# Kernel optimization log

Measured on AMD Instinct MI355X. Metric: run time of the kernel, lower is better.

The kernel has to match this reference:

```python
import jax, jax.numpy as jnp
import numpy as np

EPS = 1e-5


def bn(x, g, b, m, v):
    # eval-mode BatchNorm2d: x [B,C,H,W], params [C]
    s = g / jnp.sqrt(v + EPS)
    return x * s[None, :, None, None] + (b - m * s)[None, :, None, None]


def conv1x1(x, w):
    # x [B,C,H,W], w [O,C]
    return jnp.einsum('bchw,oc->bohw', x, w)


def offset_conv(x, w, b):
    # 3x3 conv, stride 1, pad 1, with bias; x [B,C,H,W], w [18,C,3,3]
    y = jax.lax.conv_general_dilated(x, w, window_strides=(1, 1),
                                     padding=((1, 1), (1, 1)),
                                     dimension_numbers=('NCHW', 'OIHW', 'NCHW'))
    return y + b[None, :, None, None]


def deform_conv3x3(x, offset, w):
    # DeformConv v1: x [B,C,H,W], offset [B,18,H,W] ((dy,dx) pairs per kernel
    # point, torchvision layout), w [O,C,3,3]; stride=1, pad=1, dil=1.
    B, C, H, W = x.shape
    oy = offset[:, 0::2]  # [B,9,H,W]
    ox = offset[:, 1::2]  # [B,9,H,W]
    kgy = (jnp.arange(9) // 3 - 1).astype(x.dtype)  # kernel y offsets
    kgx = (jnp.arange(9) % 3 - 1).astype(x.dtype)   # kernel x offsets
    hh = jnp.arange(H, dtype=x.dtype)
    ww = jnp.arange(W, dtype=x.dtype)
    py = hh[None, None, :, None] + kgy[None, :, None, None] + oy  # [B,9,H,W]
    px = ww[None, None, None, :] + kgx[None, :, None, None] + ox  # [B,9,H,W]
    feat = jnp.transpose(x, (0, 2, 3, 1))  # [B,H,W,C]
    y0 = jnp.floor(py)
    x0 = jnp.floor(px)
    wy = py - y0
    wx = px - x0
    bidx = jnp.arange(B).reshape(B, 1, 1, 1)
    acc = jnp.zeros((B, 9, H, W, C), dtype=x.dtype)
    for dy in (0, 1):
        for dx in (0, 1):
            yi = y0 + dy
            xi = x0 + dx
            wgt = (wy if dy else 1.0 - wy) * (wx if dx else 1.0 - wx)
            valid = (yi >= 0) & (yi <= H - 1) & (xi >= 0) & (xi <= W - 1)
            yic = jnp.clip(yi, 0, H - 1).astype(jnp.int32)
            xic = jnp.clip(xi, 0, W - 1).astype(jnp.int32)
            g = feat[bidx, yic, xic]  # gather -> [B,9,H,W,C]
            acc = acc + (wgt * valid.astype(x.dtype))[..., None] * g
    wk = w.reshape(w.shape[0], C, 9)  # k = ky*3+kx matches kgy/kgx order
    return jnp.einsum('bkhwc,ock->bohw', acc, wk)


def setup_inputs() -> dict:
    key = jax.random.key(0)
    ks = jax.random.split(key, 20)
    B, Cin, H, W = 16, 1024, 32, 32
    P, O = 256, 1024  # width / outplanes
    f32 = jnp.float32
    d = {}
    d['x'] = jax.random.normal(ks[0], (B, Cin, H, W), f32)
    d['w1'] = jax.random.normal(ks[1], (P, Cin), f32) * 0.02
    d['bn1_g'] = 1.0 + 0.1 * jax.random.normal(ks[2], (P,), f32)
    d['bn1_b'] = 0.1 * jax.random.normal(ks[3], (P,), f32)
    d['bn1_m'] = 0.1 * jax.random.normal(ks[4], (P,), f32)
    d['bn1_v'] = 0.5 + jax.random.uniform(ks[5], (P,), f32)
    d['off_w'] = jax.random.normal(ks[6], (18, P, 3, 3), f32) * 0.01
    d['off_b'] = 0.01 * jax.random.normal(ks[7], (18,), f32)
    d['w2'] = jax.random.normal(ks[8], (P, P, 3, 3), f32) * 0.02
    d['bn2_g'] = 1.0 + 0.1 * jax.random.normal(ks[9], (P,), f32)
    d['bn2_b'] = 0.1 * jax.random.normal(ks[10], (P,), f32)
    d['bn2_m'] = 0.1 * jax.random.normal(ks[11], (P,), f32)
    d['bn2_v'] = 0.5 + jax.random.uniform(ks[12], (P,), f32)
    d['w3'] = jax.random.normal(ks[13], (O, P), f32) * 0.02
    d['bn3_g'] = 1.0 + 0.1 * jax.random.normal(ks[14], (O,), f32)
    d['bn3_b'] = 0.1 * jax.random.normal(ks[15], (O,), f32)
    d['bn3_m'] = 0.1 * jax.random.normal(ks[16], (O,), f32)
    d['bn3_v'] = 0.5 + jax.random.uniform(ks[17], (O,), f32)
    return d


def reference(x, w1, bn1_g, bn1_b, bn1_m, bn1_v, off_w, off_b, w2,
              bn2_g, bn2_b, bn2_m, bn2_v, w3, bn3_g, bn3_b, bn3_m, bn3_v):
    shortcut = x
    h = jax.nn.relu(bn(conv1x1(x, w1), bn1_g, bn1_b, bn1_m, bn1_v))
    offset = offset_conv(h, off_w, off_b)
    h = deform_conv3x3(h, offset, w2)
    h = jax.nn.relu(bn(h, bn2_g, bn2_b, bn2_m, bn2_v))
    h = bn(conv1x1(h, w3), bn3_g, bn3_b, bn3_m, bn3_v)
    return jax.nn.relu(h + shortcut)
```

## Files before the change

### kernel.cpp

```cpp
#include <hip/hip_runtime.h>

#define BN_EPS 1e-5f

typedef __bf16 bf16_t;
typedef __bf16 bf16x8 __attribute__((ext_vector_type(8)));
typedef float f32x4 __attribute__((ext_vector_type(4)));


__global__ void __launch_bounds__(1024) k_bnprep(
    const float* g1, const float* b1, const float* m1, const float* v1,
    const float* g2, const float* b2, const float* m2, const float* v2,
    const float* g3, const float* b3, const float* m3, const float* v3,
    float* bnc) {
    int t = threadIdx.x;
    if (t < 256) {
        float s = g1[t] * rsqrtf(v1[t] + BN_EPS);
        bnc[t] = s;
        bnc[256 + t] = b1[t] - m1[t] * s;
        float s2 = g2[t] * rsqrtf(v2[t] + BN_EPS);
        bnc[512 + t] = s2;
        bnc[768 + t] = b2[t] - m2[t] * s2;
    }
    float s3 = g3[t] * rsqrtf(v3[t] + BN_EPS);
    bnc[1024 + t] = s3;
    bnc[2048 + t] = b3[t] - m3[t] * s3;
}

__global__ void __launch_bounds__(256) k_cast(const float* __restrict__ s,
                                              bf16_t* __restrict__ d, int n4) {
    int i = blockIdx.x * 256 + threadIdx.x;
    if (i >= n4) return;
    float4 v = ((const float4*)s)[i];
    d[4 * i + 0] = (bf16_t)v.x;
    d[4 * i + 1] = (bf16_t)v.y;
    d[4 * i + 2] = (bf16_t)v.z;
    d[4 * i + 3] = (bf16_t)v.w;
}

__global__ void __launch_bounds__(256) k_w2b(const float* __restrict__ w2,
                                             bf16_t* __restrict__ w2t) {
    int i = blockIdx.x * 256 + threadIdx.x;
    int o = i / 2304;
    int r = i - o * 2304;
    int kk = r >> 8;
    int c = r & 255;
    w2t[i] = (bf16_t)w2[(size_t)o * 2304 + c * 9 + kk];
}

__global__ void __launch_bounds__(256) k_owtb(const float* __restrict__ ow,
                                              bf16_t* __restrict__ owtb) {
    int idx = blockIdx.x * 256 + threadIdx.x;
    if (idx >= 73728) return;
    int j = idx / 2304;
    int rem = idx - j * 2304;
    int kp = rem >> 8;
    int c = rem & 255;
    float v = (j < 18) ? ow[(j * 256 + c) * 9 + kp] : 0.f;
    owtb[idx] = (bf16_t)v;
}

__global__ void __launch_bounds__(256) k_xb(const float* __restrict__ x,
                                            bf16_t* __restrict__ xb) {
    __shared__ float ld[64 * 68];
    int t = threadIdx.x;
    int hw0 = blockIdx.x * 64, c0 = blockIdx.y * 64, b = blockIdx.z;
    int ci = t >> 2, h0 = (t & 3) * 16;
    const float* src = x + ((size_t)(b * 1024 + c0 + ci) << 10) + hw0 + h0;
#pragma unroll
    for (int i = 0; i < 4; ++i)
        *(float4*)(ld + ci * 68 + h0 + 4 * i) = *(const float4*)(src + 4 * i);
    __syncthreads();
    int r = t >> 2, cc0 = (t & 3) * 16;
    bf16x8 o0, o1;
#pragma unroll
    for (int i = 0; i < 8; ++i) o0[i] = (bf16_t)ld[(cc0 + i) * 68 + r];
#pragma unroll
    for (int i = 0; i < 8; ++i) o1[i] = (bf16_t)ld[(cc0 + 8 + i) * 68 + r];
    bf16_t* dst = xb + ((size_t)(b * 1024 + hw0 + r) << 10) + c0 + cc0;
    *(bf16x8*)dst = o0;
    *(bf16x8*)(dst + 8) = o1;
}

__global__ void __launch_bounds__(256) k_gemm64(
    const bf16_t* __restrict__ A, const bf16_t* __restrict__ Bt, int K, int ldo,
    const float* __restrict__ sc, const float* __restrict__ sh,
    const float* __restrict__ resid, bf16_t* __restrict__ outb,
    float* __restrict__ outf, int epi) {
    __shared__ __align__(16) bf16_t As[64 * 40];
    __shared__ __align__(16) bf16_t Bs[128 * 40];
    int t = threadIdx.x;
    int lane = t & 63;
    int w = t >> 6;
    int wm = w >> 1, wn = w & 1;
    int m0 = blockIdx.x * 64, n0 = blockIdx.y * 128;

    int ar = t >> 2, as_ = t & 3;
    const bf16_t* ag = A + (size_t)(m0 + ar) * K + as_ * 8;
    int aw = ar * 40 + ((as_ ^ (ar & 3)) * 8);
    int bn0 = t >> 2, bs_ = t & 3;
    const bf16_t* bg0 = Bt + (size_t)(n0 + bn0) * K + bs_ * 8;
    const bf16_t* bg1 = Bt + (size_t)(n0 + 64 + bn0) * K + bs_ * 8;
    int bw0 = bn0 * 40 + ((bs_ ^ (bn0 & 3)) * 8);
    int bw1 = (64 + bn0) * 40 + ((bs_ ^ (bn0 & 3)) * 8);

    int asel = lane >> 4;
    int ar0 = wm * 32 + (lane & 15);
    int aoff0 = ar0 * 40 + ((asel ^ (ar0 & 3)) * 8);
    int aoff1 = (ar0 + 16) * 40 + ((asel ^ (ar0 & 3)) * 8);
    int boff[4];
#pragma unroll
    for (int ni = 0; ni < 4; ++ni) {
        int n = wn * 64 + ni * 16 + (lane & 15);
        boff[ni] = n * 40 + ((asel ^ (n & 3)) * 8);
    }
    f32x4 acc[2][4] = {};

    for (int k0 = 0; k0 < K; k0 += 32) {
        __syncthreads();
        *(bf16x8*)(As + aw) = *(const bf16x8*)(ag + k0);
        *(bf16x8*)(Bs + bw0) = *(const bf16x8*)(bg0 + k0);
        *(bf16x8*)(Bs + bw1) = *(const bf16x8*)(bg1 + k0);
        __syncthreads();
        bf16x8 a0 = *(const bf16x8*)(As + aoff0);
        bf16x8 a1 = *(const bf16x8*)(As + aoff1);
#pragma unroll
        for (int ni = 0; ni < 4; ++ni) {
            bf16x8 bv = *(const bf16x8*)(Bs + boff[ni]);
            acc[0][ni] = __builtin_amdgcn_mfma_f32_16x16x32_bf16(a0, bv, acc[0][ni], 0, 0, 0);
            acc[1][ni] = __builtin_amdgcn_mfma_f32_16x16x32_bf16(a1, bv, acc[1][ni], 0, 0, 0);
        }
    }

    int mrb = m0 + wm * 32 + (lane >> 4) * 4;
    int ncb = n0 + wn * 64 + (lane & 15);
    if (epi == 0) {
#pragma unroll
        for (int mi = 0; mi < 2; ++mi)
#pragma unroll
            for (int ni = 0; ni < 4; ++ni) {
                int n = ncb + ni * 16;
                float s = sc[n], h = sh[n];
#pragma unroll
                for (int j = 0; j < 4; ++j) {
                    int m = mrb + mi * 16 + j;
                    float v = fmaxf(fmaf(acc[mi][ni][j], s, h), 0.f);
                    outb[(size_t)m * ldo + n] = (bf16_t)v;
                }
            }
    } else {
#pragma unroll
        for (int mi = 0; mi < 2; ++mi) {
            int m = mrb + mi * 16;
            int bb = m >> 10, hw = m & 1023;
#pragma unroll
            for (int ni = 0; ni < 4; ++ni) {
                int o = ncb + ni * 16;
                float s = sc[o], h = sh[o];
                size_t idx = (((size_t)(bb * 1024 + o)) << 10) + hw;
                float4 r = *(const float4*)(resid + idx);
                float4 v;
                v.x = fmaxf(fmaf(acc[mi][ni][0], s, h) + r.x, 0.f);
                v.y = fmaxf(fmaf(acc[mi][ni][1], s, h) + r.y, 0.f);
                v.z = fmaxf(fmaf(acc[mi][ni][2], s, h) + r.z, 0.f);
                v.w = fmaxf(fmaf(acc[mi][ni][3], s, h) + r.w, 0.f);
                *(float4*)(outf + idx) = v;
            }
        }
    }
}

__global__ void __launch_bounds__(256) k_off(const bf16_t* __restrict__ h1,
                                             const bf16_t* __restrict__ owtb,
                                             const float* __restrict__ offb,
                                             float* __restrict__ off) {
    int t = threadIdx.x;
    int lane = t & 63;
    int w = t >> 6;
    int mi = w >> 1, ni = w & 1;
    int y = blockIdx.x, b = blockIdx.y;
    int x = (lane & 15) + mi * 16;
    int ksel = lane >> 4;
    int j = (lane & 15) + ni * 16;
    f32x4 acc = {};
    const bf16_t* h1base = h1 + ((size_t)b << 18);
    const bf16_t* brow = owtb + (size_t)j * 2304 + ksel * 8;

    for (int kp = 0; kp < 9; ++kp) {
        int yy = y + kp / 3 - 1;
        int xx = x + kp % 3 - 1;
        bool vy = (yy >= 0) && (yy < 32);
        bool vx = (xx >= 0) && (xx < 32);
        const bf16_t* arow = h1base + (((size_t)(yy * 32 + xx)) << 8) + ksel * 8;
        const bf16_t* bp = brow + kp * 256;
#pragma unroll
        for (int s = 0; s < 8; ++s) {
            bf16x8 av = {};
            if (vy && vx) av = *(const bf16x8*)(arow + s * 32);
            bf16x8 bv = *(const bf16x8*)(bp + s * 32);
            acc = __builtin_amdgcn_mfma_f32_16x16x32_bf16(av, bv, acc, 0, 0, 0);
        }
    }
    if (j < 18) {
        float bias = offb[j];
        size_t ob = (size_t)b * 18432 + (size_t)j * 1024 + y * 32 + mi * 16;
#pragma unroll
        for (int r = 0; r < 4; ++r) {
            off[ob + ksel * 4 + r] = acc[r] + bias;
        }
    }
}

__global__ void __launch_bounds__(256) k_deform(const bf16_t* __restrict__ h1,
                                                const float* __restrict__ off,
                                                const bf16_t* __restrict__ w2t,
                                                const float* __restrict__ bnc,
                                                bf16_t* __restrict__ h2) {
    __shared__ __align__(16) bf16_t As[32 * 264];
    __shared__ __align__(16) bf16_t Bs[256 * 40];
    int t = threadIdx.x;
    int lane = t & 63;
    int wn = t >> 6;
    int y = blockIdx.x, b = blockIdx.y;
    int sx = t >> 3, scg = t & 7;
    int bn0 = t >> 2, bs_ = t & 3;
    int asel = lane >> 4;
    int ar0 = lane & 15;
    int boff[4];
#pragma unroll
    for (int ni = 0; ni < 4; ++ni) {
        int n = wn * 64 + ni * 16 + (lane & 15);
        boff[ni] = n * 40 + ((asel ^ (n & 3)) * 8);
    }
    f32x4 acc[2][4] = {};
    size_t obase = (size_t)b * 18432 + (size_t)y * 32 + sx;
    size_t h1row = (size_t)b * 1024;

    for (int k = 0; k < 9; ++k) {
        __syncthreads();
        float oy = off[obase + (size_t)(2 * k) * 1024];
        float ox = off[obase + (size_t)(2 * k + 1) * 1024];
        float py = (float)y + (float)(k / 3 - 1) + oy;
        float px = (float)sx + (float)(k % 3 - 1) + ox;
        float fy = floorf(py), fx = floorf(px);
        float wy = py - fy, wx = px - fx;
        int y0 = (int)fy, x0 = (int)fx;
        int y1 = y0 + 1, x1 = x0 + 1;
        float vy0 = (y0 >= 0 && y0 < 32) ? 1.f : 0.f;
        float vy1 = (y1 >= 0 && y1 < 32) ? 1.f : 0.f;
        float vx0 = (x0 >= 0 && x0 < 32) ? 1.f : 0.f;
        float vx1 = (x1 >= 0 && x1 < 32) ? 1.f : 0.f;
        int yc0 = min(max(y0, 0), 31), yc1 = min(max(y1, 0), 31);
        int xc0 = min(max(x0, 0), 31), xc1 = min(max(x1, 0), 31);
        float w00 = (1.f - wy) * (1.f - wx) * vy0 * vx0;
        float w01 = (1.f - wy) * wx * vy0 * vx1;
        float w10 = wy * (1.f - wx) * vy1 * vx0;
        float w11 = wy * wx * vy1 * vx1;
        const bf16_t* p00 = h1 + ((h1row + yc0 * 32 + xc0) << 8);
        const bf16_t* p01 = h1 + ((h1row + yc0 * 32 + xc1) << 8);
        const bf16_t* p10 = h1 + ((h1row + yc1 * 32 + xc0) << 8);
        const bf16_t* p11 = h1 + ((h1row + yc1 * 32 + xc1) << 8);
#pragma unroll
        for (int q = 0; q < 4; ++q) {
            int c = scg * 32 + q * 8;
            bf16x8 v00 = *(const bf16x8*)(p00 + c);
            bf16x8 v01 = *(const bf16x8*)(p01 + c);
            bf16x8 v10 = *(const bf16x8*)(p10 + c);
            bf16x8 v11 = *(const bf16x8*)(p11 + c);
            bf16x8 r;
#pragma unroll
            for (int e = 0; e < 8; ++e) {
                float f = w00 * (float)v00[e] + w01 * (float)v01[e] +
                          w10 * (float)v10[e] + w11 * (float)v11[e];
                r[e] = (bf16_t)f;
            }
            int slot = scg * 4 + q;
            int slotx = (slot & ~3) | ((slot & 3) ^ (sx & 3));
            *(bf16x8*)(As + sx * 264 + slotx * 8) = r;
        }
        for (int c0 = 0; c0 < 256; c0 += 32) {
            __syncthreads();
            const bf16_t* wg = w2t + (size_t)k * 256 + c0 + bs_ * 8;
#pragma unroll
            for (int j = 0; j < 4; ++j) {
                int n = j * 64 + bn0;
                *(bf16x8*)(Bs + n * 40 + ((bs_ ^ (n & 3)) * 8)) =
                    *(const bf16x8*)(wg + (size_t)n * 2304);
            }
            __syncthreads();
            int sbase = c0 >> 3;
            bf16x8 a0 = *(const bf16x8*)(As + ar0 * 264 + (sbase + (asel ^ (ar0 & 3))) * 8);
            bf16x8 a1 = *(const bf16x8*)(As + (ar0 + 16) * 264 + (sbase + (asel ^ (ar0 & 3))) * 8);
#pragma unroll
            for (int ni = 0; ni < 4; ++ni) {
                bf16x8 bv = *(const bf16x8*)(Bs + boff[ni]);
                acc[0][ni] = __builtin_amdgcn_mfma_f32_16x16x32_bf16(a0, bv, acc[0][ni], 0, 0, 0);
                acc[1][ni] = __builtin_amdgcn_mfma_f32_16x16x32_bf16(a1, bv, acc[1][ni], 0, 0, 0);
            }
        }
    }
    int mrb = (lane >> 4) * 4;
    int ncb = wn * 64 + (lane & 15);
#pragma unroll
    for (int mi = 0; mi < 2; ++mi)
#pragma unroll
        for (int ni = 0; ni < 4; ++ni) {
            int n = ncb + ni * 16;
            float s = bnc[512 + n], h = bnc[768 + n];
#pragma unroll
            for (int j = 0; j < 4; ++j) {
                int row = mrb + mi * 16 + j;
                float v = fmaxf(fmaf(acc[mi][ni][j], s, h), 0.f);
                h2[(((size_t)(b * 1024 + y * 32 + row)) << 8) + n] = (bf16_t)v;
            }
        }
}

extern "C" void kernel_launch(void* const* d_in, const int* in_sizes, int n_in,
                              void* d_out, int out_size, void* d_ws, size_t ws_size,
                              hipStream_t stream) {
    const float* x = (const float*)d_in[0];
    const float* w1 = (const float*)d_in[1];
    const float* bn1g = (const float*)d_in[2];
    const float* bn1b = (const float*)d_in[3];
    const float* bn1m = (const float*)d_in[4];
    const float* bn1v = (const float*)d_in[5];
    const float* off_w = (const float*)d_in[6];
    const float* off_b = (const float*)d_in[7];
    const float* w2 = (const float*)d_in[8];
    const float* bn2g = (const float*)d_in[9];
    const float* bn2b = (const float*)d_in[10];
    const float* bn2m = (const float*)d_in[11];
    const float* bn2v = (const float*)d_in[12];
    const float* w3 = (const float*)d_in[13];
    const float* bn3g = (const float*)d_in[14];
    const float* bn3b = (const float*)d_in[15];
    const float* bn3m = (const float*)d_in[16];
    const float* bn3v = (const float*)d_in[17];
    float* out = (float*)d_out;

    char* ws = (char*)d_ws;
    float* bnc = (float*)(ws + 0);
    bf16_t* owtb = (bf16_t*)(ws + 12288);
    float* off = (float*)(ws + 178176);
    bf16_t* xb = (bf16_t*)(ws + 1357824);
    bf16_t* w1b = (bf16_t*)(ws + 34912256);
    bf16_t* w2tb = (bf16_t*)(ws + 35436544);
    bf16_t* w3b = (bf16_t*)(ws + 36616192);
    bf16_t* h1b = (bf16_t*)(ws + 37140480);
    bf16_t* h2b = (bf16_t*)(ws + 45529088);

    k_bnprep<<<1, 1024, 0, stream>>>(bn1g, bn1b, bn1m, bn1v, bn2g, bn2b, bn2m,
                                     bn2v, bn3g, bn3b, bn3m, bn3v, bnc);
    k_cast<<<256, 256, 0, stream>>>(w1, w1b, 65536);
    k_cast<<<256, 256, 0, stream>>>(w3, w3b, 65536);
    k_w2b<<<2304, 256, 0, stream>>>(w2, w2tb);
    k_owtb<<<288, 256, 0, stream>>>(off_w, owtb);
    k_xb<<<dim3(16, 16, 16), 256, 0, stream>>>(x, xb);
    k_gemm64<<<dim3(256, 2), 256, 0, stream>>>(xb, w1b, 1024, 256, bnc,
                                               bnc + 256, nullptr, h1b, nullptr, 0);
    k_off<<<dim3(32, 16), 256, 0, stream>>>(h1b, owtb, off_b, off);
    k_deform<<<dim3(32, 16), 256, 0, stream>>>(h1b, off, w2tb, bnc, h2b);
    k_gemm64<<<dim3(256, 8), 256, 0, stream>>>(h2b, w3b, 256, 1024, bnc + 1024,
                                               bnc + 2048, x, nullptr, out, 1);
}
```

Baseline: 357.4 us.

## Load deform-conv weights directly from global memory instead of staging through LDS

Removes the shared-memory staging of the w2 weight tile in the deformable conv kernel. Each lane now reads its B fragment straight from global memory (expected to hit L2), so the per-32-channel inner loop no longer needs two block barriers. The sampled-input tile is re-laid out into 8 swizzled panels of 32x40 so one barrier per kernel point is enough. The cost is more global loads per MFMA, which could stall on latency.

```diff
diff --git a/kernel.cpp b/kernel.cpp
--- a/kernel.cpp
+++ b/kernel.cpp
@@ -215,21 +215,21 @@
                                                 const bf16_t* __restrict__ w2t,
                                                 const float* __restrict__ bnc,
                                                 bf16_t* __restrict__ h2) {
-    __shared__ __align__(16) bf16_t As[32 * 264];
-    __shared__ __align__(16) bf16_t Bs[256 * 40];
+    __shared__ __align__(16) bf16_t As[8 * 1288];
     int t = threadIdx.x;
     int lane = t & 63;
     int wn = t >> 6;
     int y = blockIdx.x, b = blockIdx.y;
     int sx = t >> 3, scg = t & 7;
-    int bn0 = t >> 2, bs_ = t & 3;
     int asel = lane >> 4;
     int ar0 = lane & 15;
-    int boff[4];
+    int aoff0 = ar0 * 40 + ((asel ^ (ar0 & 3)) * 8);
+    int aoff1 = (ar0 + 16) * 40 + ((asel ^ ((ar0 + 16) & 3)) * 8);
+    const bf16_t* br[4];
 #pragma unroll
     for (int ni = 0; ni < 4; ++ni) {
         int n = wn * 64 + ni * 16 + (lane & 15);
-        boff[ni] = n * 40 + ((asel ^ (n & 3)) * 8);
+        br[ni] = w2t + (size_t)n * 2304 + asel * 8;
     }
     f32x4 acc[2][4] = {};
     size_t obase = (size_t)b * 18432 + (size_t)y * 32 + sx;
@@ -259,6 +259,7 @@
         const bf16_t* p01 = h1 + ((h1row + yc0 * 32 + xc1) << 8);
         const bf16_t* p10 = h1 + ((h1row + yc1 * 32 + xc0) << 8);
         const bf16_t* p11 = h1 + ((h1row + yc1 * 32 + xc1) << 8);
+        bf16_t* pnl = As + scg * 1288 + sx * 40;
 #pragma unroll
         for (int q = 0; q < 4; ++q) {
             int c = scg * 32 + q * 8;
@@ -273,26 +274,19 @@
                           w10 * (float)v10[e] + w11 * (float)v11[e];
                 r[e] = (bf16_t)f;
             }
-            int slot = scg * 4 + q;
-            int slotx = (slot & ~3) | ((slot & 3) ^ (sx & 3));
-            *(bf16x8*)(As + sx * 264 + slotx * 8) = r;
-        }
-        for (int c0 = 0; c0 < 256; c0 += 32) {
-            __syncthreads();
-            const bf16_t* wg = w2t + (size_t)k * 256 + c0 + bs_ * 8;
-#pragma unroll
-            for (int j = 0; j < 4; ++j) {
-                int n = j * 64 + bn0;
-                *(bf16x8*)(Bs + n * 40 + ((bs_ ^ (n & 3)) * 8)) =
-                    *(const bf16x8*)(wg + (size_t)n * 2304);
-            }
-            __syncthreads();
-            int sbase = c0 >> 3;
-            bf16x8 a0 = *(const bf16x8*)(As + ar0 * 264 + (sbase + (asel ^ (ar0 & 3))) * 8);
-            bf16x8 a1 = *(const bf16x8*)(As + (ar0 + 16) * 264 + (sbase + (asel ^ (ar0 & 3))) * 8);
+            *(bf16x8*)(pnl + ((q ^ (sx & 3)) * 8)) = r;
+        }
+        __syncthreads();
+        const bf16_t* wb = w2t ? (const bf16_t*)0 : (const bf16_t*)0; (void)wb;
+#pragma unroll
+        for (int p = 0; p < 8; ++p) {
+            const bf16_t* pb = As + p * 1288;
+            bf16x8 a0 = *(const bf16x8*)(pb + aoff0);
+            bf16x8 a1 = *(const bf16x8*)(pb + aoff1);
+            int ko = k * 256 + p * 32;
 #pragma unroll
             for (int ni = 0; ni < 4; ++ni) {
-                bf16x8 bv = *(const bf16x8*)(Bs + boff[ni]);
+                bf16x8 bv = *(const bf16x8*)(br[ni] + ko);
                 acc[0][ni] = __builtin_amdgcn_mfma_f32_16x16x32_bf16(a0, bv, acc[0][ni], 0, 0, 0);
                 acc[1][ni] = __builtin_amdgcn_mfma_f32_16x16x32_bf16(a1, bv, acc[1][ni], 0, 0, 0);
             }
```

Measured after the change: 352.9 us. About the same (-1.3%).
